# Optimization experiments

Measured on AMD Instinct MI355X. Metric: run time of the kernel, lower is better.

## Reference

```python
import math
import jax, jax.numpy as jnp
import numpy as np

HEADS, HD = 16, 64  # head_dim = hidden_size // num_heads = 1024 // 16

def _c(a):
    # a: [2, ...] stacked (real, imag) -> complex64
    return jax.lax.complex(a[0], a[1])

def setup_inputs() -> dict:
    key = jax.random.key(0)
    ks = jax.random.split(key, 16)
    B, S, L, H = 2, 2048, 2048, 1024  # batch, chunk len, cache len, hidden
    w_scale = 1.0 / math.sqrt(2 * H)  # complex fan-in scaling
    d = {
        "hidden":  jax.random.normal(ks[0], (2, B, S, H), jnp.float32),
        "k_cache": jax.random.normal(ks[1], (2, B, L, HEADS, HD), jnp.float32),
        "v_cache": jax.random.normal(ks[2], (2, B, L, HEADS, HD), jnp.float32),
        "qw": jax.random.normal(ks[3], (2, H, H), jnp.float32) * w_scale,
        "qb": jax.random.normal(ks[4], (2, H), jnp.float32) * 0.01,
        "kw": jax.random.normal(ks[5], (2, H, H), jnp.float32) * w_scale,
        "kb": jax.random.normal(ks[6], (2, H), jnp.float32) * 0.01,
        "vw": jax.random.normal(ks[7], (2, H, H), jnp.float32) * w_scale,
        "vb": jax.random.normal(ks[8], (2, H), jnp.float32) * 0.01,
        "ow": jax.random.normal(ks[9], (2, H, H), jnp.float32) * w_scale,
        "ob": jax.random.normal(ks[10], (2, H), jnp.float32) * 0.01,
        "ln_gamma": jnp.stack([jnp.ones(H, jnp.float32) + 0.01 * jax.random.normal(ks[11], (H,)),
                               0.01 * jax.random.normal(ks[12], (H,))]),
        "ln_beta":  0.01 * jax.random.normal(ks[13], (2, H), jnp.float32),
    }
    return d

def _complex_layernorm(x, gamma, beta, eps=1e-5):
    mu = jnp.mean(x, axis=-1, keepdims=True)              # complex mean
    xc = x - mu
    var = jnp.mean(xc.real**2 + xc.imag**2, axis=-1, keepdims=True)
    return xc / jnp.sqrt(var + eps) * gamma + beta

def _clin(z, w, b):
    # complex linear: z [..., in] @ W^T [out, in] + b [out]
    return jnp.einsum('bsh,oh->bso', z, _c(w)) + _c(b)

def reference(hidden, k_cache, v_cache, qw, qb, kw, kb, vw, vb, ow, ob, ln_gamma, ln_beta):
    x = _c(hidden)                                        # [B,S,H] complex64
    B, S, H = x.shape
    normed = _complex_layernorm(x, _c(ln_gamma), _c(ln_beta))
    Q = _clin(normed, qw, qb).reshape(B, S, HEADS, HD)
    K_new = _clin(normed, kw, kb).reshape(B, S, HEADS, HD)
    V_new = _clin(normed, vw, vb).reshape(B, S, HEADS, HD)
    K = jnp.concatenate([_c(k_cache), K_new], axis=1)     # [B, L+S, nh, hd]
    V = jnp.concatenate([_c(v_cache), V_new], axis=1)
    cache_len = k_cache.shape[2]
    kv = K.shape[1]                                       # == window_size here
    # Hermitian score: Re(Q K^dagger) / sqrt(hd)
    scores = jnp.einsum('bqhd,bkhd->bhqk', Q, jnp.conj(K)).real / math.sqrt(HD)
    row = jnp.arange(S)[:, None]
    col = jnp.arange(kv)[None, :]
    # prefix (cache) fully visible; causal within the new chunk
    mask = jnp.where((col >= cache_len) & (col - cache_len > row), -jnp.inf, 0.0).astype(scores.dtype)
    w = jax.nn.softmax(scores + mask[None, None], axis=-1)  # real weights
    out = jax.lax.complex(jnp.einsum('bhqk,bkhd->bqhd', w, V.real),
                          jnp.einsum('bhqk,bkhd->bqhd', w, V.imag)).reshape(B, S, H)
    delta = _clin(out, ow, ob)
    y = x + delta
    out_stacked = jnp.stack([y.real, y.imag])             # [2,B,S,H]
    new_k = jnp.stack([K.real, K.imag])                   # [2,B,window,nh,hd]
    new_v = jnp.stack([V.real, V.imag])
    return (out_stacked, new_k, new_v)
```

## Files before the change

### kernel.cpp

```cpp
#include <hip/hip_runtime.h>

#define HEADS 16
#define SEQ   2048
#define HID   1024
#define CACHE 2048
#define KVLEN 4096
#define MROWS 4096
#define KD    2048

typedef float  f32x4  __attribute__((ext_vector_type(4)));
typedef __bf16 bf16x4 __attribute__((ext_vector_type(4)));
typedef __bf16 bf16x8 __attribute__((ext_vector_type(8)));

__device__ __forceinline__ void gload_lds16(const void* g, void* l) {
  __builtin_amdgcn_global_load_lds((const __attribute__((address_space(1))) void*)g,
                                   (__attribute__((address_space(3))) void*)l, 16, 0, 0);
}

__global__ __launch_bounds__(256) void k_layernorm(const float* __restrict__ hid,
                                                   const float* __restrict__ gamma,
                                                   const float* __restrict__ beta,
                                                   __bf16* __restrict__ normed) {
  int row = blockIdx.x;
  int t = threadIdx.x;
  const float* xr = hid + (size_t)row * HID;
  const float* xi = hid + (size_t)MROWS * HID + (size_t)row * HID;
  float vr[4], vi[4];
  float sr = 0.f, si = 0.f;
#pragma unroll
  for (int i = 0; i < 4; i++) { int h = t + i * 256; vr[i] = xr[h]; vi[i] = xi[h]; sr += vr[i]; si += vi[i]; }
  __shared__ float red[2][4];
  for (int m = 1; m < 64; m <<= 1) { sr += __shfl_xor(sr, m); si += __shfl_xor(si, m); }
  int wid = t >> 6, l = t & 63;
  if (l == 0) { red[0][wid] = sr; red[1][wid] = si; }
  __syncthreads();
  float mr = (red[0][0] + red[0][1] + red[0][2] + red[0][3]) * (1.0f / HID);
  float mi = (red[1][0] + red[1][1] + red[1][2] + red[1][3]) * (1.0f / HID);
  float sv = 0.f;
#pragma unroll
  for (int i = 0; i < 4; i++) { float a = vr[i] - mr, b = vi[i] - mi; sv += a * a + b * b; }
  for (int m = 1; m < 64; m <<= 1) sv += __shfl_xor(sv, m);
  __syncthreads();
  if (l == 0) red[0][wid] = sv;
  __syncthreads();
  float var = (red[0][0] + red[0][1] + red[0][2] + red[0][3]) * (1.0f / HID);
  float inv = rsqrtf(var + 1e-5f);
  __bf16* outr = normed + (size_t)row * KD;
#pragma unroll
  for (int i = 0; i < 4; i++) {
    int h = t + i * 256;
    float a = (vr[i] - mr) * inv, b = (vi[i] - mi) * inv;
    float gr = gamma[h], gi = gamma[HID + h], br = beta[h], bi = beta[HID + h];
    outr[h]       = (__bf16)(a * gr - b * gi + br);
    outr[HID + h] = (__bf16)(a * gi + b * gr + bi);
  }
}

__global__ __launch_bounds__(256) void k_packw(const float* __restrict__ qw, const float* __restrict__ kw,
                                               const float* __restrict__ vw, const float* __restrict__ ow,
                                               __bf16* __restrict__ dst) {
  int idx = blockIdx.x * 256 + threadIdx.x;
  int sel = idx >> 19;
  int li  = idx & 524287;
  const float* w = sel == 0 ? qw : (sel == 1 ? kw : (sel == 2 ? vw : ow));
  int o  = li >> 8;
  int k0 = (li & 255) * 8;
  const float* wr = w;
  const float* wi = w + HID * HID;
  int oimag = (o >= HID);
  int oo = o & (HID - 1);
  bf16x8 v;
#pragma unroll
  for (int j = 0; j < 8; j++) {
    int k = k0 + j;
    int kim = (k >= HID);
    int kk = k & (HID - 1);
    float x;
    if (!oimag) x = kim ? -wi[oo * HID + kk] : wr[oo * HID + kk];
    else        x = kim ?  wr[oo * HID + kk] : wi[oo * HID + kk];
    v[j] = (__bf16)x;
  }
  *(bf16x8*)(dst + ((size_t)sel << 22) + (size_t)o * KD + k0) = v;
}

__global__ __launch_bounds__(256) void k_copyk(const float* __restrict__ kc,
                                               float* __restrict__ nk,
                                               __bf16* __restrict__ Ka) {
  int li = blockIdx.x * 256 + threadIdx.x;
  int c4 = li & 255;
  int kv = (li >> 8) & 2047;
  int b  = (li >> 19) & 1;
  int p  = (li >> 20) & 1;
  f32x4 v = *(const f32x4*)(kc + (((size_t)((p * 2 + b) * 2048 + kv)) << 10) + c4 * 4);
  *(f32x4*)(nk + ((((size_t)(p * 2 + b)) * KVLEN + kv) << 10) + c4 * 4) = v;
  int h = c4 >> 4, d = (c4 & 15) * 4;
  bf16x4 w;
#pragma unroll
  for (int j = 0; j < 4; j++) w[j] = (__bf16)v[j];
  *(bf16x4*)(Ka + (((size_t)(b * 16 + h)) * KVLEN + kv) * 128 + p * 64 + d) = w;
}

__global__ __launch_bounds__(256) void k_buildv(const float* __restrict__ vc,
                                                float* __restrict__ nv,
                                                __bf16* __restrict__ dst) {
  __shared__ float tile[32][129];
  int kt = blockIdx.x;
  int bh = blockIdx.y;
  int b = bh >> 4, h = bh & 15;
  int t = threadIdx.x;
  int kv0 = kt * 32;
#pragma unroll
  for (int i = 0; i < 16; i++) {
    int idx = i * 256 + t;
    int kvl = idx >> 7, dsl = idx & 127;
    int p = dsl >> 6, d = dsl & 63;
    float v = vc[(((size_t)(p * 2 + b)) * CACHE + kv0 + kvl) * HID + h * 64 + d];
    tile[kvl][dsl] = v;
    nv[(((size_t)(p * 2 + b)) * KVLEN + kv0 + kvl) * HID + h * 64 + d] = v;
  }
  __syncthreads();
#pragma unroll
  for (int i = 0; i < 16; i++) {
    int idx = i * 256 + t;
    int dsl = idx >> 5, kvl = idx & 31;
    dst[(((size_t)bh) * 128 + dsl) * KVLEN + kv0 + kvl] = (__bf16)tile[kvl][dsl];
  }
}

#define BM 128
#define BN 128
#define BK 64
template <int QKV>
__global__ __launch_bounds__(256, 3) void k_gemm(const __bf16* __restrict__ A,
                                                 const __bf16* __restrict__ Bp,
                                                 const float* __restrict__ bias0,
                                                 const float* __restrict__ bias1,
                                                 const float* __restrict__ bias2,
                                                 const float* __restrict__ hid,
                                                 float* __restrict__ outF0,
                                                 float* __restrict__ outF1,
                                                 __bf16* __restrict__ outB0,
                                                 __bf16* __restrict__ outB1,
                                                 __bf16* __restrict__ outB2) {
  __shared__ __align__(16) __bf16 As[BM * BK];
  __shared__ __align__(16) __bf16 Bs[BN * BK];
  int bm0 = blockIdx.x * BM, bn0 = blockIdx.y * BN;
  int t = threadIdx.x, l = t & 63, wid = t >> 6;
  int wr = wid >> 1, wc = wid & 1;
  int l15 = l & 15, lg = l >> 4;
  f32x4 acc[4][4];
  f32x4 zero = {0.f, 0.f, 0.f, 0.f};
#pragma unroll
  for (int i = 0; i < 4; i++)
#pragma unroll
    for (int j = 0; j < 4; j++) acc[i][j] = zero;
  const __bf16* Ab = A + (size_t)bm0 * KD;
  const __bf16* Bb = Bp + (size_t)bn0 * KD;
  for (int k0 = 0; k0 < KD; k0 += BK) {
#pragma unroll
    for (int c = 0; c < 4; c++) {
      int idx = c * 256 + t;
      int row = idx >> 3, ch = idx & 7;
      int chs = ch ^ (row & 7);
      gload_lds16(Ab + (size_t)row * KD + k0 + chs * 8, As + idx * 8);
      gload_lds16(Bb + (size_t)row * KD + k0 + chs * 8, Bs + idx * 8);
    }
    __syncthreads();
#pragma unroll
    for (int ks = 0; ks < 2; ks++) {
      bf16x8 af[4], bfv[4];
#pragma unroll
      for (int i = 0; i < 4; i++) {
        int ra = wr * 64 + i * 16 + l15;
        int rb = wc * 64 + i * 16 + l15;
        af[i]  = *(const bf16x8*)((const char*)As + ra * 128 + ((ks * 64 + lg * 16) ^ ((ra & 7) << 4)));
        bfv[i] = *(const bf16x8*)((const char*)Bs + rb * 128 + ((ks * 64 + lg * 16) ^ ((rb & 7) << 4)));
      }
#pragma unroll
      for (int mi = 0; mi < 4; mi++)
#pragma unroll
        for (int ni = 0; ni < 4; ni++)
          acc[mi][ni] = __builtin_amdgcn_mfma_f32_16x16x32_bf16(af[mi], bfv[ni], acc[mi][ni], 0, 0, 0);
    }
    __syncthreads();
  }
#pragma unroll
  for (int mi = 0; mi < 4; mi++) {
#pragma unroll
    for (int ni = 0; ni < 4; ni++) {
      int mbase = bm0 + wr * 64 + mi * 16 + lg * 4;
      int n = bn0 + wc * 64 + ni * 16 + l15;
      int b = mbase >> 11, sbase = mbase & 2047;
      if (QKV) {
        int mode = n >> 11, nl = n & 2047;
        const float* bias = mode == 0 ? bias0 : (mode == 1 ? bias1 : bias2);
        float bv = bias[nl];
        int p = nl >> 10, hd = nl & 1023;
        if (mode == 2) {
          bf16x4 w;
#pragma unroll
          for (int j = 0; j < 4; j++) {
            float v = acc[mi][ni][j] + bv;
            outF1[(((size_t)(p * 2 + b)) * KVLEN + (CACHE + sbase + j)) * HID + hd] = v;
            w[j] = (__bf16)v;
          }
          *(bf16x4*)(outB2 + (((size_t)(b * 16 + (hd >> 6))) * 128 + p * 64 + (hd & 63)) * KVLEN + CACHE + sbase) = w;
        } else {
#pragma unroll
          for (int j = 0; j < 4; j++) {
            float v = acc[mi][ni][j] + bv;
            int s = sbase + j;
            if (mode == 0) {
              outB0[(((size_t)(b * 16 + (hd >> 6))) * SEQ + s) * 128 + p * 64 + (hd & 63)] = (__bf16)v;
            } else {
              outF0[(((size_t)(p * 2 + b)) * KVLEN + (CACHE + s)) * HID + hd] = v;
              outB1[(((size_t)(b * 16 + (hd >> 6))) * KVLEN + (CACHE + s)) * 128 + p * 64 + (hd & 63)] = (__bf16)v;
            }
          }
        }
      } else {
        float bv = bias0[n];
        int p = n >> 10;
#pragma unroll
        for (int j = 0; j < 4; j++) {
          float v = acc[mi][ni][j] + bv;
          size_t off = (((size_t)(p * 2 + b)) * SEQ + (sbase + j)) * HID + (n & 1023);
          outF0[off] = v + hid[off];
        }
      }
    }
  }
}

__global__ __launch_bounds__(256, 2) void k_attn(const __bf16* __restrict__ Q,
                                                 const __bf16* __restrict__ Kt,
                                                 const __bf16* __restrict__ Vt,
                                                 __bf16* __restrict__ outp) {
  __shared__ __align__(16) __bf16 Ks[2][64 * 128];
  __shared__ __align__(16) __bf16 Vs[2][128 * 64];
  __shared__ __align__(16) __bf16 Ps[4][32 * 64];
  int id = blockIdx.y * gridDim.x + blockIdx.x;
  int xcd = id & 7, li = id >> 3;
  int bh = (xcd << 2) | (li >> 4);
  int ql = li & 15;
  int qt = (ql & 1) ? (15 - (ql >> 1)) : (ql >> 1);
  int b = bh >> 4, h = bh & 15;
  int t = threadIdx.x, l = t & 63, wid = t >> 6;
  int l15 = l & 15, lg = l >> 4;
  const __bf16* Qb = Q + ((size_t)bh * SEQ) * 128;
  const __bf16* Kb = Kt + ((size_t)bh * KVLEN) * 128;
  const __bf16* Vb = Vt + ((size_t)bh * 128) * KVLEN;
  __bf16* Pw = &Ps[wid][0];
  int q0 = qt * 128 + wid * 32;
  bf16x8 aQ[2][4];
#pragma unroll
  for (int mi = 0; mi < 2; mi++)
#pragma unroll
    for (int dk = 0; dk < 4; dk++)
      aQ[mi][dk] = *(const bf16x8*)(Qb + (size_t)(q0 + mi * 16 + l15) * 128 + dk * 32 + lg * 8);
  f32x4 zero = {0.f, 0.f, 0.f, 0.f};
  f32x4 o[2][8];
  f32x4 sums[2];
#pragma unroll
  for (int mi = 0; mi < 2; mi++) {
    sums[mi] = zero;
#pragma unroll
    for (int df = 0; df < 8; df++) o[mi][df] = zero;
  }
  bf16x8 ones;
#pragma unroll
  for (int i = 0; i < 8; i++) ones[i] = (__bf16)1.0f;
  const int nfull = 32 + 2 * qt;
  const int nt = nfull + 2;
  int sw = (l15 & 7) << 4;

  auto STAGE = [&](int bb, int ti) {
    int kv0 = ti * 64;
#pragma unroll
    for (int c = 0; c < 4; c++) {
      int idx = c * 256 + t;
      int kr = idx >> 4;
      gload_lds16(Kb + (size_t)(kv0 + kr) * 128 + (((idx & 15) ^ (kr & 7)) << 3), &Ks[bb][idx * 8]);
      int vr = idx >> 3;
      gload_lds16(Vb + (size_t)vr * KVLEN + kv0 + (((idx & 7) ^ (vr & 7)) << 3), &Vs[bb][idx * 8]);
    }
  };

  STAGE(0, 0);
  for (int ti = 0; ti < nt; ti++) {
    int bb = ti & 1;
    if (ti + 1 < nt) {
      STAGE(bb ^ 1, ti + 1);
      asm volatile("s_waitcnt vmcnt(8)" ::: "memory");
    } else {
      asm volatile("s_waitcnt vmcnt(0)" ::: "memory");
    }
    __builtin_amdgcn_s_barrier();
    const char* KsB = (const char*)&Ks[bb][0];
    const char* VsB = (const char*)&Vs[bb][0];
    f32x4 sacc[2][4];
    __builtin_amdgcn_s_setprio(1);
#pragma unroll
    for (int kvf = 0; kvf < 4; kvf++) {
      sacc[0][kvf] = zero; sacc[1][kvf] = zero;
      const char* kbase = KsB + (kvf * 16 + l15) * 256;
#pragma unroll
      for (int dk = 0; dk < 4; dk++) {
        bf16x8 bK = *(const bf16x8*)(kbase + ((dk * 64 + lg * 16) ^ sw));
        sacc[0][kvf] = __builtin_amdgcn_mfma_f32_16x16x32_bf16(bK, aQ[0][dk], sacc[0][kvf], 0, 0, 0);
        sacc[1][kvf] = __builtin_amdgcn_mfma_f32_16x16x32_bf16(bK, aQ[1][dk], sacc[1][kvf], 0, 0, 0);
      }
    }
    __builtin_amdgcn_s_setprio(0);
    bool masked = (ti >= nfull);
#pragma unroll
    for (int mi = 0; mi < 2; mi++) {
      int row = mi * 16 + l15;
      int rx = (row & 7) << 3;
#pragma unroll
      for (int kvf = 0; kvf < 4; kvf++) {
        bf16x4 w;
#pragma unroll
        for (int j = 0; j < 4; j++) {
          float p = exp2f(sacc[mi][kvf][j] * 0.18033688011112042f);
          if (masked) {
            int cg = ti * 64 + kvf * 16 + lg * 4 + j - CACHE;
            if (cg > qt * 128 + wid * 32 + row) p = 0.f;
          }
          w[j] = (__bf16)p;
        }
        *(bf16x4*)(Pw + row * 64 + ((kvf * 16 + lg * 4) ^ rx)) = w;
      }
    }
    bf16x8 bV[2][8], aP[2][2];
#pragma unroll
    for (int ks = 0; ks < 2; ks++) {
      int off = (ks * 64 + lg * 16) ^ sw;
#pragma unroll
      for (int df = 0; df < 8; df++)
        bV[ks][df] = *(const bf16x8*)(VsB + (df * 16 + l15) * 128 + off);
    }
#pragma unroll
    for (int mi = 0; mi < 2; mi++) {
      int row = mi * 16 + l15;
      int rx = (row & 7) << 3;
      const __bf16* pb = Pw + row * 64;
#pragma unroll
      for (int ks = 0; ks < 2; ks++)
        aP[mi][ks] = *(const bf16x8*)(pb + ((ks * 32 + lg * 8) ^ rx));
    }
    __builtin_amdgcn_s_setprio(1);
#pragma unroll
    for (int mi = 0; mi < 2; mi++) {
#pragma unroll
      for (int ks = 0; ks < 2; ks++) {
        sums[mi] = __builtin_amdgcn_mfma_f32_16x16x32_bf16(aP[mi][ks], ones, sums[mi], 0, 0, 0);
#pragma unroll
        for (int df = 0; df < 8; df++)
          o[mi][df] = __builtin_amdgcn_mfma_f32_16x16x32_bf16(aP[mi][ks], bV[ks][df], o[mi][df], 0, 0, 0);
      }
    }
    __builtin_amdgcn_s_setprio(0);
    __builtin_amdgcn_s_barrier();
  }
#pragma unroll
  for (int mi = 0; mi < 2; mi++) {
    float inv[4];
#pragma unroll
    for (int j = 0; j < 4; j++) inv[j] = 1.0f / sums[mi][j];
#pragma unroll
    for (int df = 0; df < 8; df++) {
      int dslot = df * 16 + l15;
      int col = (dslot < 64) ? (h * 64 + dslot) : (1024 + h * 64 + (dslot - 64));
#pragma unroll
      for (int j = 0; j < 4; j++) {
        int qg2 = q0 + mi * 16 + lg * 4 + j;
        float v = o[mi][df][j] * inv[j];
        outp[((size_t)(b * SEQ + qg2)) * KD + col] = (__bf16)v;
      }
    }
  }
}

extern "C" void kernel_launch(void* const* d_in, const int* in_sizes, int n_in,
                              void* d_out, int out_size, void* d_ws, size_t ws_size,
                              hipStream_t stream) {
  const float* hid = (const float*)d_in[0];
  const float* kc  = (const float*)d_in[1];
  const float* vc  = (const float*)d_in[2];
  const float* qw  = (const float*)d_in[3];
  const float* qb  = (const float*)d_in[4];
  const float* kw  = (const float*)d_in[5];
  const float* kb  = (const float*)d_in[6];
  const float* vw  = (const float*)d_in[7];
  const float* vb  = (const float*)d_in[8];
  const float* ow  = (const float*)d_in[9];
  const float* ob  = (const float*)d_in[10];
  const float* lg  = (const float*)d_in[11];
  const float* lb  = (const float*)d_in[12];

  float* y  = (float*)d_out;
  float* nk = y + 8388608;
  float* nv = nk + 16777216;

  char* ws = (char*)d_ws;
  __bf16* normed = (__bf16*)(ws);
  __bf16* wall   = (__bf16*)(ws + 16777216);
  __bf16* Qa     = (__bf16*)(ws + 50331648);
  __bf16* Ka     = (__bf16*)(ws + 67108864);
  __bf16* Va     = (__bf16*)(ws + 100663296);
  __bf16* ao     = (__bf16*)(ws + 134217728);

  k_layernorm<<<4096, 256, 0, stream>>>(hid, lg, lb, normed);
  k_packw<<<8192, 256, 0, stream>>>(qw, kw, vw, ow, wall);
  k_copyk<<<8192, 256, 0, stream>>>(kc, nk, Ka);
  dim3 gv(64, 32);
  k_buildv<<<gv, 256, 0, stream>>>(vc, nv, Va);
  dim3 gq(32, 48);
  k_gemm<1><<<gq, 256, 0, stream>>>(normed, wall, qb, kb, vb, nullptr, nk, nv, Qa, Ka, Va);
  dim3 ga(16, 32);
  k_attn<<<ga, 256, 0, stream>>>(Qa, Ka, Va, ao);
  dim3 go(32, 16);
  k_gemm<0><<<go, 256, 0, stream>>>(ao, wall + ((size_t)3 << 22), ob, nullptr, nullptr, hid, y, nullptr, nullptr, nullptr, nullptr);
}
```

Measured before the change: 433.5 us.

## Halve attention query tile and drop LDS double buffering for higher occupancy

The attention kernel now gives each block 64 query rows (16 per wave) instead of 128, doubling the grid, and targets 4 blocks per CU instead of 2. K/V staging goes from a double-buffered prefetch to one buffer with a full wait before each tile, which cuts LDS and registers. The goal is to hide latency through more resident waves. In exchange, each K/V tile is reused by half as many queries, so global/L2 traffic doubles and the load-compute overlap inside a block is lost.

```diff
diff --git a/kernel.cpp b/kernel.cpp
--- a/kernel.cpp
+++ b/kernel.cpp
@@ -232,18 +232,18 @@
   }
 }
 
-__global__ __launch_bounds__(256, 2) void k_attn(const __bf16* __restrict__ Q,
+__global__ __launch_bounds__(256, 4) void k_attn(const __bf16* __restrict__ Q,
                                                  const __bf16* __restrict__ Kt,
                                                  const __bf16* __restrict__ Vt,
                                                  __bf16* __restrict__ outp) {
-  __shared__ __align__(16) __bf16 Ks[2][64 * 128];
-  __shared__ __align__(16) __bf16 Vs[2][128 * 64];
-  __shared__ __align__(16) __bf16 Ps[4][32 * 64];
+  __shared__ __align__(16) __bf16 Ks[64 * 128];
+  __shared__ __align__(16) __bf16 Vs[128 * 64];
+  __shared__ __align__(16) __bf16 Ps[4][16 * 64];
   int id = blockIdx.y * gridDim.x + blockIdx.x;
   int xcd = id & 7, li = id >> 3;
-  int bh = (xcd << 2) | (li >> 4);
-  int ql = li & 15;
-  int qt = (ql & 1) ? (15 - (ql >> 1)) : (ql >> 1);
+  int bh = (xcd << 2) | (li >> 5);
+  int ql = li & 31;
+  int qt = (ql & 1) ? (31 - (ql >> 1)) : (ql >> 1);
   int b = bh >> 4, h = bh & 15;
   int t = threadIdx.x, l = t & 63, wid = t >> 6;
   int l15 = l & 15, lg = l >> 4;
@@ -251,133 +251,99 @@
   const __bf16* Kb = Kt + ((size_t)bh * KVLEN) * 128;
   const __bf16* Vb = Vt + ((size_t)bh * 128) * KVLEN;
   __bf16* Pw = &Ps[wid][0];
-  int q0 = qt * 128 + wid * 32;
-  bf16x8 aQ[2][4];
-#pragma unroll
-  for (int mi = 0; mi < 2; mi++)
-#pragma unroll
-    for (int dk = 0; dk < 4; dk++)
-      aQ[mi][dk] = *(const bf16x8*)(Qb + (size_t)(q0 + mi * 16 + l15) * 128 + dk * 32 + lg * 8);
+  int q0 = qt * 64 + wid * 16;
+  bf16x8 aQ[4];
+#pragma unroll
+  for (int dk = 0; dk < 4; dk++)
+    aQ[dk] = *(const bf16x8*)(Qb + (size_t)(q0 + l15) * 128 + dk * 32 + lg * 8);
   f32x4 zero = {0.f, 0.f, 0.f, 0.f};
-  f32x4 o[2][8];
-  f32x4 sums[2];
-#pragma unroll
-  for (int mi = 0; mi < 2; mi++) {
-    sums[mi] = zero;
-#pragma unroll
-    for (int df = 0; df < 8; df++) o[mi][df] = zero;
-  }
+  f32x4 o[8];
+  f32x4 sums = zero;
+#pragma unroll
+  for (int df = 0; df < 8; df++) o[df] = zero;
   bf16x8 ones;
 #pragma unroll
   for (int i = 0; i < 8; i++) ones[i] = (__bf16)1.0f;
-  const int nfull = 32 + 2 * qt;
-  const int nt = nfull + 2;
+  const int nfull = 32 + qt;
+  const int nt = nfull + 1;
   int sw = (l15 & 7) << 4;
-
-  auto STAGE = [&](int bb, int ti) {
+  int row = l15;
+  int rx = (row & 7) << 3;
+
+  for (int ti = 0; ti < nt; ti++) {
     int kv0 = ti * 64;
 #pragma unroll
     for (int c = 0; c < 4; c++) {
       int idx = c * 256 + t;
       int kr = idx >> 4;
-      gload_lds16(Kb + (size_t)(kv0 + kr) * 128 + (((idx & 15) ^ (kr & 7)) << 3), &Ks[bb][idx * 8]);
+      gload_lds16(Kb + (size_t)(kv0 + kr) * 128 + (((idx & 15) ^ (kr & 7)) << 3), Ks + idx * 8);
       int vr = idx >> 3;
-      gload_lds16(Vb + (size_t)vr * KVLEN + kv0 + (((idx & 7) ^ (vr & 7)) << 3), &Vs[bb][idx * 8]);
-    }
-  };
-
-  STAGE(0, 0);
-  for (int ti = 0; ti < nt; ti++) {
-    int bb = ti & 1;
-    if (ti + 1 < nt) {
-      STAGE(bb ^ 1, ti + 1);
-      asm volatile("s_waitcnt vmcnt(8)" ::: "memory");
-    } else {
-      asm volatile("s_waitcnt vmcnt(0)" ::: "memory");
-    }
+      gload_lds16(Vb + (size_t)vr * KVLEN + kv0 + (((idx & 7) ^ (vr & 7)) << 3), Vs + idx * 8);
+    }
+    asm volatile("s_waitcnt vmcnt(0)" ::: "memory");
     __builtin_amdgcn_s_barrier();
-    const char* KsB = (const char*)&Ks[bb][0];
-    const char* VsB = (const char*)&Vs[bb][0];
-    f32x4 sacc[2][4];
+    f32x4 sacc[4];
     __builtin_amdgcn_s_setprio(1);
 #pragma unroll
     for (int kvf = 0; kvf < 4; kvf++) {
-      sacc[0][kvf] = zero; sacc[1][kvf] = zero;
-      const char* kbase = KsB + (kvf * 16 + l15) * 256;
+      sacc[kvf] = zero;
+      const char* kbase = (const char*)Ks + (kvf * 16 + l15) * 256;
 #pragma unroll
       for (int dk = 0; dk < 4; dk++) {
         bf16x8 bK = *(const bf16x8*)(kbase + ((dk * 64 + lg * 16) ^ sw));
-        sacc[0][kvf] = __builtin_amdgcn_mfma_f32_16x16x32_bf16(bK, aQ[0][dk], sacc[0][kvf], 0, 0, 0);
-        sacc[1][kvf] = __builtin_amdgcn_mfma_f32_16x16x32_bf16(bK, aQ[1][dk], sacc[1][kvf], 0, 0, 0);
+        sacc[kvf] = __builtin_amdgcn_mfma_f32_16x16x32_bf16(bK, aQ[dk], sacc[kvf], 0, 0, 0);
       }
     }
     __builtin_amdgcn_s_setprio(0);
     bool masked = (ti >= nfull);
 #pragma unroll
-    for (int mi = 0; mi < 2; mi++) {
-      int row = mi * 16 + l15;
-      int rx = (row & 7) << 3;
-#pragma unroll
-      for (int kvf = 0; kvf < 4; kvf++) {
-        bf16x4 w;
-#pragma unroll
-        for (int j = 0; j < 4; j++) {
-          float p = exp2f(sacc[mi][kvf][j] * 0.18033688011112042f);
-          if (masked) {
-            int cg = ti * 64 + kvf * 16 + lg * 4 + j - CACHE;
-            if (cg > qt * 128 + wid * 32 + row) p = 0.f;
-          }
-          w[j] = (__bf16)p;
+    for (int kvf = 0; kvf < 4; kvf++) {
+      bf16x4 w;
+#pragma unroll
+      for (int j = 0; j < 4; j++) {
+        float p = exp2f(sacc[kvf][j] * 0.18033688011112042f);
+        if (masked) {
+          if (kvf * 16 + lg * 4 + j > wid * 16 + row) p = 0.f;
         }
-        *(bf16x4*)(Pw + row * 64 + ((kvf * 16 + lg * 4) ^ rx)) = w;
+        w[j] = (__bf16)p;
       }
-    }
-    bf16x8 bV[2][8], aP[2][2];
+      *(bf16x4*)(Pw + row * 64 + ((kvf * 16 + lg * 4) ^ rx)) = w;
+    }
+    bf16x8 bV[2][8], aP[2];
 #pragma unroll
     for (int ks = 0; ks < 2; ks++) {
       int off = (ks * 64 + lg * 16) ^ sw;
 #pragma unroll
       for (int df = 0; df < 8; df++)
-        bV[ks][df] = *(const bf16x8*)(VsB + (df * 16 + l15) * 128 + off);
-    }
-#pragma unroll
-    for (int mi = 0; mi < 2; mi++) {
-      int row = mi * 16 + l15;
-      int rx = (row & 7) << 3;
-      const __bf16* pb = Pw + row * 64;
-#pragma unroll
-      for (int ks = 0; ks < 2; ks++)
-        aP[mi][ks] = *(const bf16x8*)(pb + ((ks * 32 + lg * 8) ^ rx));
-    }
+        bV[ks][df] = *(const bf16x8*)((const char*)Vs + (df * 16 + l15) * 128 + off);
+    }
+    const __bf16* pb = Pw + row * 64;
+#pragma unroll
+    for (int ks = 0; ks < 2; ks++)
+      aP[ks] = *(const bf16x8*)(pb + ((ks * 32 + lg * 8) ^ rx));
     __builtin_amdgcn_s_setprio(1);
 #pragma unroll
-    for (int mi = 0; mi < 2; mi++) {
-#pragma unroll
-      for (int ks = 0; ks < 2; ks++) {
-        sums[mi] = __builtin_amdgcn_mfma_f32_16x16x32_bf16(aP[mi][ks], ones, sums[mi], 0, 0, 0);
-#pragma unroll
-        for (int df = 0; df < 8; df++)
-          o[mi][df] = __builtin_amdgcn_mfma_f32_16x16x32_bf16(aP[mi][ks], bV[ks][df], o[mi][df], 0, 0, 0);
-      }
+    for (int ks = 0; ks < 2; ks++) {
+      sums = __builtin_amdgcn_mfma_f32_16x16x32_bf16(aP[ks], ones, sums, 0, 0, 0);
+#pragma unroll
+      for (int df = 0; df < 8; df++)
+        o[df] = __builtin_amdgcn_mfma_f32_16x16x32_bf16(aP[ks], bV[ks][df], o[df], 0, 0, 0);
     }
     __builtin_amdgcn_s_setprio(0);
     __builtin_amdgcn_s_barrier();
   }
-#pragma unroll
-  for (int mi = 0; mi < 2; mi++) {
-    float inv[4];
-#pragma unroll
-    for (int j = 0; j < 4; j++) inv[j] = 1.0f / sums[mi][j];
-#pragma unroll
-    for (int df = 0; df < 8; df++) {
-      int dslot = df * 16 + l15;
-      int col = (dslot < 64) ? (h * 64 + dslot) : (1024 + h * 64 + (dslot - 64));
-#pragma unroll
-      for (int j = 0; j < 4; j++) {
-        int qg2 = q0 + mi * 16 + lg * 4 + j;
-        float v = o[mi][df][j] * inv[j];
-        outp[((size_t)(b * SEQ + qg2)) * KD + col] = (__bf16)v;
-      }
+  float inv[4];
+#pragma unroll
+  for (int j = 0; j < 4; j++) inv[j] = 1.0f / sums[j];
+#pragma unroll
+  for (int df = 0; df < 8; df++) {
+    int dslot = df * 16 + l15;
+    int col = (dslot < 64) ? (h * 64 + dslot) : (1024 + h * 64 + (dslot - 64));
+#pragma unroll
+    for (int j = 0; j < 4; j++) {
+      int qg2 = q0 + lg * 4 + j;
+      float v = o[df][j] * inv[j];
+      outp[((size_t)(b * SEQ + qg2)) * KD + col] = (__bf16)v;
     }
   }
 }
@@ -418,7 +384,7 @@
   k_buildv<<<gv, 256, 0, stream>>>(vc, nv, Va);
   dim3 gq(32, 48);
   k_gemm<1><<<gq, 256, 0, stream>>>(normed, wall, qb, kb, vb, nullptr, nk, nv, Qa, Ka, Va);
-  dim3 ga(16, 32);
+  dim3 ga(32, 32);
   k_attn<<<ga, 256, 0, stream>>>(Qa, Ka, Va, ao);
   dim3 go(32, 16);
   k_gemm<0><<<go, 256, 0, stream>>>(ao, wall + ((size_t)3 << 22), ob, nullptr, nullptr, hid, y, nullptr, nullptr, nullptr, nullptr);
```

After: 746.2 us. 1.72x slower.
